# Performance work log

Measured on AMD Instinct MI355X. Metric: run time of the kernel, lower is better.

Reference implementation:

```python
import jax, jax.numpy as jnp
import numpy as np

B, S, H, NH = 2, 2048, 1024, 16
HD = H // NH            # 64
ROT = HD // 2           # rotary dim = 32
COND, FF = 1024, 4 * H
BASE = 10000.0
EPS = 1e-5


def setup_inputs() -> dict:
    key = jax.random.key(0)
    ks = jax.random.split(key, 16)
    w = lambda k, shape: jax.random.normal(k, shape, dtype=jnp.float32) * 0.02
    z = lambda shape: jnp.zeros(shape, dtype=jnp.float32)
    o = lambda shape: jnp.ones(shape, dtype=jnp.float32)
    return {
        'x': jax.random.normal(ks[0], (B, S, H), dtype=jnp.float32),
        'cond': jax.random.normal(ks[1], (B, COND), dtype=jnp.float32),
        'attn_mask': jnp.ones((B, S), dtype=bool),
        'wq': w(ks[2], (H, H)), 'bq': z((H,)),
        'wk': w(ks[3], (H, H)), 'bk': z((H,)),
        'wv': w(ks[4], (H, H)), 'bv': z((H,)),
        'wo': w(ks[5], (H, H)), 'bo': z((H,)),
        'ln1_g': o((H,)), 'ln1_b': z((H,)),
        'ada1_w': w(ks[6], (COND, 2 * H)), 'ada1_b': z((2 * H,)),
        'ln2_g': o((H,)), 'ln2_b': z((H,)),
        'ada2_w': w(ks[7], (COND, 2 * H)), 'ada2_b': z((2 * H,)),
        'ff_w1': w(ks[8], (H, FF)), 'ff_b1': z((FF,)),
        'ff_w2': w(ks[9], (FF, H)), 'ff_b2': z((H,)),
    }


def _layer_norm(x, g, b):
    mu = jnp.mean(x, axis=-1, keepdims=True)
    var = jnp.mean(jnp.square(x - mu), axis=-1, keepdims=True)
    return (x - mu) * jax.lax.rsqrt(var + EPS) * g + b


def _ada_norm(x, cond, g, b, w, bw):
    shift, scale = jnp.split(cond @ w + bw, 2, axis=-1)  # each [B,H]
    return _layer_norm(x, g, b) * (1.0 + scale[:, None, :]) + shift[:, None, :]


def _rotary_sin_cos(seq_len):
    inv_freq = 1.0 / (BASE ** (jnp.arange(ROT, dtype=jnp.float32) / ROT))
    freqs = jnp.arange(seq_len, dtype=jnp.float32)[:, None] * inv_freq[None, :]  # [S,ROT]
    return jnp.sin(freqs), jnp.cos(freqs)


def _apply_rotary(x, sin, cos):
    # x: [B,NH,S,HD]; sin/cos: [S,ROT] broadcast over batch/heads
    xe, xo = x[..., ::2], x[..., 1::2]
    re = xe * cos - xo * sin
    ro = xo * cos + xe * sin
    return jnp.stack((re, ro), axis=-1).reshape(x.shape)


def _split_heads(x):
    b, s, _ = x.shape
    return x.reshape(b, s, NH, HD).transpose(0, 2, 1, 3)  # [B,NH,S,HD]


def reference(x, cond, attn_mask, wq, bq, wk, bk, wv, bv, wo, bo,
              ln1_g, ln1_b, ada1_w, ada1_b, ln2_g, ln2_b, ada2_w, ada2_b,
              ff_w1, ff_b1, ff_w2, ff_b2):
    residual = x
    h = _ada_norm(x, cond, ln1_g, ln1_b, ada1_w, ada1_b)
    q = _split_heads(h @ wq + bq)
    k = _split_heads(h @ wk + bk)
    v = _split_heads(h @ wv + bv)
    sin, cos = _rotary_sin_cos(x.shape[1])
    q = _apply_rotary(q, sin, cos)
    k = _apply_rotary(k, sin, cos)
    scores = jnp.einsum('bhqd,bhkd->bhqk', q, k) / np.sqrt(HD).astype(np.float32)
    scores = jnp.where(attn_mask[:, None, None, :], scores, -jnp.inf)
    attn = jax.nn.softmax(scores, axis=-1)
    out = jnp.einsum('bhqk,bhkd->bhqd', attn, v)
    out = out.transpose(0, 2, 1, 3).reshape(x.shape[0], x.shape[1], H)
    x = residual + out @ wo + bo
    residual = x
    h = _ada_norm(x, cond, ln2_g, ln2_b, ada2_w, ada2_b)
    ff = jax.nn.gelu(h @ ff_w1 + ff_b1, approximate=False) @ ff_w2 + ff_b2
    return residual + ff
```

## Files before the change

### kernel.cpp

```cpp
#include <hip/hip_runtime.h>
#include <cstdint>

#define B_DIM 2
#define S_DIM 2048
#define H_DIM 1024
#define NHEAD 16
#define HDIM 64
#define FF_DIM 4096
#define M_DIM (B_DIM*S_DIM)

typedef __bf16 bf16;
typedef _Float16 f16;
typedef __bf16 bf16x8 __attribute__((ext_vector_type(8)));
typedef __bf16 bf16x4 __attribute__((ext_vector_type(4)));
typedef _Float16 f16x4 __attribute__((ext_vector_type(4)));
typedef __fp16 fp16x2_raw __attribute__((ext_vector_type(2)));
typedef float  f32x4  __attribute__((ext_vector_type(4)));

#define QK_SCALE 0.18033688011112042f

#if __has_builtin(__builtin_amdgcn_exp2f)
#define EXP2F(x) __builtin_amdgcn_exp2f(x)
#else
#define EXP2F(x) __expf(0.69314718055994531f*(x))
#endif

#define ATOMIC_FADD(p, v) __hip_atomic_fetch_add((p), (v), __ATOMIC_RELAXED, __HIP_MEMORY_SCOPE_AGENT)

__device__ __forceinline__ void g2l16(void* lds, const void* g) {
    __builtin_amdgcn_global_load_lds(
        (const __attribute__((address_space(1))) void*)g,
        (__attribute__((address_space(3))) void*)lds,
        16, 0, 0);
}

__global__ __launch_bounds__(256) void wtrans_all(const float* __restrict__ wq,
                                                  const float* __restrict__ wk,
                                                  const float* __restrict__ wv,
                                                  const float* __restrict__ wo,
                                                  const float* __restrict__ fw1,
                                                  const float* __restrict__ fw2,
                                                  bf16* __restrict__ wqkv,
                                                  bf16* __restrict__ wto,
                                                  bf16* __restrict__ wtf1,
                                                  bf16* __restrict__ wtf2,
                                                  float* __restrict__ adao) {
    __shared__ float t[32][33];
    int tt = blockIdx.x;
    if (tt >= 12288) {
        int i = (tt - 12288) * 1024 + threadIdx.x * 4;
        ((float4*)(adao + i))[0] = (float4){0.f, 0.f, 0.f, 0.f};
        return;
    }
    const float* in; bf16* out; int R, C, base, shift;
    if (tt < 4096) {
        int j = tt >> 10; base = tt & 1023; R = 1024; C = 1024; shift = 5;
        in  = (j == 0) ? wq : (j == 1) ? wk : (j == 2) ? wv : wo;
        out = (j < 3) ? (wqkv + (size_t)j * 1024 * 1024) : wto;
    } else if (tt < 8192) {
        base = tt - 4096; R = 1024; C = 4096; shift = 7; in = fw1; out = wtf1;
    } else {
        base = tt - 8192; R = 4096; C = 1024; shift = 5; in = fw2; out = wtf2;
    }
    int bx = base & ((1 << shift) - 1), by = base >> shift;
    int c0 = bx * 32, r0 = by * 32;
    int tx = threadIdx.x & 31, ty = threadIdx.x >> 5;
#pragma unroll
    for (int i = 0; i < 4; i++) {
        int r = ty + i * 8;
        t[r][tx] = in[(size_t)(r0 + r) * C + c0 + tx];
    }
    __syncthreads();
#pragma unroll
    for (int i = 0; i < 4; i++) {
        int cc = ty + i * 8;
        out[(size_t)(c0 + cc) * R + r0 + tx] = (bf16)t[tx][cc];
    }
}

__global__ __launch_bounds__(256) void ada_gemm(const float* __restrict__ cond,
                                                const float* __restrict__ w1, const float* __restrict__ b1,
                                                const float* __restrict__ w2, const float* __restrict__ b2,
                                                float* __restrict__ o1, float* __restrict__ o2) {
    int layer = blockIdx.y;
    const float* w    = layer ? w2 : w1;
    const float* bias = layer ? b2 : b1;
    float* o          = layer ? o2 : o1;
    int tid = threadIdx.x;
    int k0 = blockIdx.x * 16;
    f32x4 acc[2][2];
#pragma unroll
    for (int b = 0; b < 2; b++)
#pragma unroll
        for (int j = 0; j < 2; j++) acc[b][j] = (f32x4){0.f, 0.f, 0.f, 0.f};

#pragma unroll
    for (int kk = 0; kk < 16; kk++) {
        int k = k0 + kk;
        float c0 = cond[k];
        float c1 = cond[1024 + k];
        const f32x4* wr = (const f32x4*)(w + (size_t)k * 2048);
        f32x4 wa = wr[tid], wb = wr[tid + 256];
#pragma unroll
        for (int c = 0; c < 4; c++) {
            acc[0][0][c] += c0 * wa[c];
            acc[0][1][c] += c0 * wb[c];
            acc[1][0][c] += c1 * wa[c];
            acc[1][1][c] += c1 * wb[c];
        }
    }
    if (blockIdx.x == 0) {
        f32x4 ba = ((const f32x4*)bias)[tid], bb = ((const f32x4*)bias)[tid + 256];
#pragma unroll
        for (int c = 0; c < 4; c++) {
            acc[0][0][c] += ba[c]; acc[1][0][c] += ba[c];
            acc[0][1][c] += bb[c]; acc[1][1][c] += bb[c];
        }
    }
#pragma unroll
    for (int b = 0; b < 2; b++)
#pragma unroll
        for (int j = 0; j < 2; j++) {
            int col = (tid + j * 256) * 4;
#pragma unroll
            for (int c = 0; c < 4; c++)
                ATOMIC_FADD(&o[b * 2048 + col + c], acc[b][j][c]);
        }
}

__global__ __launch_bounds__(256) void adaln_k(const float* __restrict__ x,
                                               const float* __restrict__ g,
                                               const float* __restrict__ be,
                                               const float* __restrict__ ada,
                                               bf16* __restrict__ h) {
    int row = blockIdx.x;
    int b = row >> 11;
    int tid = threadIdx.x;
    float4 v = ((const float4*)(x + (size_t)row * H_DIM))[tid];
    float s = v.x + v.y + v.z + v.w;
    __shared__ float sm[4];
#pragma unroll
    for (int m = 32; m >= 1; m >>= 1) s += __shfl_xor(s, m, 64);
    if ((tid & 63) == 0) sm[tid >> 6] = s;
    __syncthreads();
    float mean = (sm[0] + sm[1] + sm[2] + sm[3]) * (1.0f / H_DIM);
    float dx = v.x - mean, dy = v.y - mean, dz = v.z - mean, dw = v.w - mean;
    float s2 = dx * dx + dy * dy + dz * dz + dw * dw;
    __syncthreads();
#pragma unroll
    for (int m = 32; m >= 1; m >>= 1) s2 += __shfl_xor(s2, m, 64);
    if ((tid & 63) == 0) sm[tid >> 6] = s2;
    __syncthreads();
    float var = (sm[0] + sm[1] + sm[2] + sm[3]) * (1.0f / H_DIM);
    float rstd = rsqrtf(var + 1e-5f);
    float4 gv = ((const float4*)g)[tid];
    float4 bv = ((const float4*)be)[tid];
    const float* shp = ada + (size_t)b * 2 * H_DIM;
    float4 shv = ((const float4*)shp)[tid];
    float4 scv = ((const float4*)(shp + H_DIM))[tid];
    bf16* hr = h + (size_t)row * H_DIM + tid * 4;
    hr[0] = (bf16)((dx * rstd * gv.x + bv.x) * (1.0f + scv.x) + shv.x);
    hr[1] = (bf16)((dy * rstd * gv.y + bv.y) * (1.0f + scv.y) + shv.y);
    hr[2] = (bf16)((dz * rstd * gv.z + bv.z) * (1.0f + scv.z) + shv.z);
    hr[3] = (bf16)((dw * rstd * gv.w + bv.w) * (1.0f + scv.w) + shv.w);
}

__global__ __launch_bounds__(256) void adaln2_fused(const float* __restrict__ x,
                                                    const float* __restrict__ bo,
                                                    const bf16* __restrict__ P0,
                                                    const bf16* __restrict__ P1,
                                                    const float* __restrict__ g,
                                                    const float* __restrict__ be,
                                                    const float* __restrict__ ada,
                                                    float* __restrict__ x2,
                                                    bf16* __restrict__ h) {
    int row = blockIdx.x;
    int b = row >> 11;
    int tid = threadIdx.x;
    float4 v = ((const float4*)(x + (size_t)row * H_DIM))[tid];
    float4 bov = ((const float4*)bo)[tid];
    bf16x4 p0 = ((const bf16x4*)(P0 + (size_t)row * H_DIM))[tid];
    bf16x4 p1 = ((const bf16x4*)(P1 + (size_t)row * H_DIM))[tid];
    v.x += bov.x + (float)p0[0] + (float)p1[0];
    v.y += bov.y + (float)p0[1] + (float)p1[1];
    v.z += bov.z + (float)p0[2] + (float)p1[2];
    v.w += bov.w + (float)p0[3] + (float)p1[3];
    ((float4*)(x2 + (size_t)row * H_DIM))[tid] = v;

    float s = v.x + v.y + v.z + v.w;
    __shared__ float sm[4];
#pragma unroll
    for (int m = 32; m >= 1; m >>= 1) s += __shfl_xor(s, m, 64);
    if ((tid & 63) == 0) sm[tid >> 6] = s;
    __syncthreads();
    float mean = (sm[0] + sm[1] + sm[2] + sm[3]) * (1.0f / H_DIM);
    float dx = v.x - mean, dy = v.y - mean, dz = v.z - mean, dw = v.w - mean;
    float s2 = dx * dx + dy * dy + dz * dz + dw * dw;
    __syncthreads();
#pragma unroll
    for (int m = 32; m >= 1; m >>= 1) s2 += __shfl_xor(s2, m, 64);
    if ((tid & 63) == 0) sm[tid >> 6] = s2;
    __syncthreads();
    float var = (sm[0] + sm[1] + sm[2] + sm[3]) * (1.0f / H_DIM);
    float rstd = rsqrtf(var + 1e-5f);
    float4 gv = ((const float4*)g)[tid];
    float4 bv = ((const float4*)be)[tid];
    const float* shp = ada + (size_t)b * 2 * H_DIM;
    float4 shv = ((const float4*)shp)[tid];
    float4 scv = ((const float4*)(shp + H_DIM))[tid];
    bf16* hr = h + (size_t)row * H_DIM + tid * 4;
    hr[0] = (bf16)((dx * rstd * gv.x + bv.x) * (1.0f + scv.x) + shv.x);
    hr[1] = (bf16)((dy * rstd * gv.y + bv.y) * (1.0f + scv.y) + shv.y);
    hr[2] = (bf16)((dz * rstd * gv.z + bv.z) * (1.0f + scv.z) + shv.z);
    hr[3] = (bf16)((dw * rstd * gv.w + bv.w) * (1.0f + scv.w) + shv.w);
}

__global__ __launch_bounds__(256) void final_reduce(const float* __restrict__ x2,
                                                    const float* __restrict__ fb2,
                                                    const bf16* __restrict__ Q,
                                                    float* __restrict__ out) {
    int i = blockIdx.x * 256 + threadIdx.x;
    float4 v = ((const float4*)x2)[i];
    float4 bv = ((const float4*)fb2)[i & 255];
    v.x += bv.x; v.y += bv.y; v.z += bv.z; v.w += bv.w;
#pragma unroll
    for (int z = 0; z < 4; z++) {
        bf16x4 q = ((const bf16x4*)(Q + (size_t)z * M_DIM * H_DIM))[i];
        v.x += (float)q[0]; v.y += (float)q[1]; v.z += (float)q[2]; v.w += (float)q[3];
    }
    ((float4*)out)[i] = v;
}

__global__ __launch_bounds__(256, 2) void gemm_bt_sp(const bf16* __restrict__ A,
                                                     const bf16* __restrict__ Bt,
                                                     bf16* __restrict__ outp,
                                                     int N, int K, int KC) {
    __shared__ bf16 As[128 * 32];
    __shared__ bf16 Bs[128 * 32];
    int m0 = blockIdx.y * 128, n0 = blockIdx.x * 128;
    int kbeg = blockIdx.z * KC, kend = kbeg + KC;
    bf16* po = outp + (size_t)blockIdx.z * M_DIM * N;
    int tid = threadIdx.x, wid = tid >> 6, lane = tid & 63;
    int quad = lane >> 4, l16 = lane & 15;
    int wm = (wid >> 1) * 64, wn = (wid & 1) * 64;

    f32x4 acc[4][4];
#pragma unroll
    for (int i = 0; i < 4; i++)
#pragma unroll
        for (int j = 0; j < 4; j++) acc[i][j] = (f32x4){0.f, 0.f, 0.f, 0.f};

    for (int k0 = kbeg; k0 < kend; k0 += 32) {
        __syncthreads();
#pragma unroll
        for (int it = 0; it < 2; it++) {
            int c = it * 256 + wid * 64 + lane;
            int row = c >> 2, kc = c & 3;
            g2l16(&As[c * 8], A  + (size_t)(m0 + row) * K + k0 + kc * 8);
            g2l16(&Bs[c * 8], Bt + (size_t)(n0 + row) * K + k0 + kc * 8);
        }
        __syncthreads();
        bf16x8 af[4], bfr[4];
#pragma unroll
        for (int i = 0; i < 4; i++) {
            af[i]  = *(const bf16x8*)&As[(wm + i * 16 + l16) * 32 + quad * 8];
            bfr[i] = *(const bf16x8*)&Bs[(wn + i * 16 + l16) * 32 + quad * 8];
        }
#pragma unroll
        for (int mt = 0; mt < 4; mt++)
#pragma unroll
            for (int nt = 0; nt < 4; nt++)
                acc[mt][nt] = __builtin_amdgcn_mfma_f32_16x16x32_bf16(af[mt], bfr[nt], acc[mt][nt], 0, 0, 0);
    }

#pragma unroll
    for (int mt = 0; mt < 4; mt++) {
#pragma unroll
        for (int nt = 0; nt < 4; nt++) {
            int col = n0 + wn + nt * 16 + l16;
#pragma unroll
            for (int r = 0; r < 4; r++) {
                int row = m0 + wm + mt * 16 + quad * 4 + r;
                po[(size_t)row * N + col] = (bf16)acc[mt][nt][r];
            }
        }
    }
}

__global__ __launch_bounds__(256, 2) void gemm_gelu(const bf16* __restrict__ A,
                                                    const bf16* __restrict__ Bt,
                                                    const float* __restrict__ bias,
                                                    bf16* __restrict__ outp,
                                                    int N, int K) {
    __shared__ bf16 As[128 * 32];
    __shared__ bf16 Bs[128 * 32];
    int m0 = blockIdx.y * 128, n0 = blockIdx.x * 128;
    int tid = threadIdx.x, wid = tid >> 6, lane = tid & 63;
    int quad = lane >> 4, l16 = lane & 15;
    int wm = (wid >> 1) * 64, wn = (wid & 1) * 64;

    f32x4 acc[4][4];
#pragma unroll
    for (int i = 0; i < 4; i++)
#pragma unroll
        for (int j = 0; j < 4; j++) acc[i][j] = (f32x4){0.f, 0.f, 0.f, 0.f};

    for (int k0 = 0; k0 < K; k0 += 32) {
        __syncthreads();
#pragma unroll
        for (int it = 0; it < 2; it++) {
            int c = it * 256 + wid * 64 + lane;
            int row = c >> 2, kc = c & 3;
            g2l16(&As[c * 8], A  + (size_t)(m0 + row) * K + k0 + kc * 8);
            g2l16(&Bs[c * 8], Bt + (size_t)(n0 + row) * K + k0 + kc * 8);
        }
        __syncthreads();
        bf16x8 af[4], bfr[4];
#pragma unroll
        for (int i = 0; i < 4; i++) {
            af[i]  = *(const bf16x8*)&As[(wm + i * 16 + l16) * 32 + quad * 8];
            bfr[i] = *(const bf16x8*)&Bs[(wn + i * 16 + l16) * 32 + quad * 8];
        }
#pragma unroll
        for (int mt = 0; mt < 4; mt++)
#pragma unroll
            for (int nt = 0; nt < 4; nt++)
                acc[mt][nt] = __builtin_amdgcn_mfma_f32_16x16x32_bf16(af[mt], bfr[nt], acc[mt][nt], 0, 0, 0);
    }

#pragma unroll
    for (int mt = 0; mt < 4; mt++) {
#pragma unroll
        for (int nt = 0; nt < 4; nt++) {
            int col = n0 + wn + nt * 16 + l16;
            float bc = bias[col];
#pragma unroll
            for (int r = 0; r < 4; r++) {
                int row = m0 + wm + mt * 16 + quad * 4 + r;
                float v = acc[mt][nt][r] + bc;
                float gl = 0.5f * v * (1.0f + erff(v * 0.70710678118654752f));
                outp[(size_t)row * N + col] = (bf16)gl;
            }
        }
    }
}

__global__ __launch_bounds__(256, 2) void gemm_qkv(const bf16* __restrict__ A,
                                                   const bf16* __restrict__ Bt,
                                                   const float* __restrict__ bq,
                                                   const float* __restrict__ bk,
                                                   const float* __restrict__ bv,
                                                   bf16* __restrict__ qr,
                                                   bf16* __restrict__ kr,
                                                   f16* __restrict__ vtf) {
    __shared__ bf16 As[128 * 32];
    __shared__ bf16 Bs[128 * 32];
    const int K = H_DIM;
    int m0 = blockIdx.y * 128, n0 = blockIdx.x * 128;
    int tid = threadIdx.x, wid = tid >> 6, lane = tid & 63;
    int quad = lane >> 4, l16 = lane & 15;
    int wm = (wid >> 1) * 64, wn = (wid & 1) * 64;

    f32x4 acc[4][4];
#pragma unroll
    for (int i = 0; i < 4; i++)
#pragma unroll
        for (int j = 0; j < 4; j++) acc[i][j] = (f32x4){0.f, 0.f, 0.f, 0.f};

    for (int k0 = 0; k0 < K; k0 += 32) {
        __syncthreads();
#pragma unroll
        for (int it = 0; it < 2; it++) {
            int c = it * 256 + wid * 64 + lane;
            int row = c >> 2, kc = c & 3;
            g2l16(&As[c * 8], A  + (size_t)(m0 + row) * K + k0 + kc * 8);
            g2l16(&Bs[c * 8], Bt + (size_t)(n0 + row) * K + k0 + kc * 8);
        }
        __syncthreads();
        bf16x8 af[4], bfr[4];
#pragma unroll
        for (int i = 0; i < 4; i++) {
            af[i]  = *(const bf16x8*)&As[(wm + i * 16 + l16) * 32 + quad * 8];
            bfr[i] = *(const bf16x8*)&Bs[(wn + i * 16 + l16) * 32 + quad * 8];
        }
#pragma unroll
        for (int mt = 0; mt < 4; mt++)
#pragma unroll
            for (int nt = 0; nt < 4; nt++)
                acc[mt][nt] = __builtin_amdgcn_mfma_f32_16x16x32_bf16(af[mt], bfr[nt], acc[mt][nt], 0, 0, 0);
    }

#pragma unroll
    for (int mt = 0; mt < 4; mt++) {
#pragma unroll
        for (int nt = 0; nt < 4; nt++) {
            int col = n0 + wn + nt * 16 + l16;
            int sec = col >> 10;
            int cc  = col & 1023;
            float bc = (sec == 0) ? bq[cc] : (sec == 1) ? bk[cc] : bv[cc];
            int hh = cc >> 6, d = cc & 63;
#pragma unroll
            for (int r = 0; r < 4; r++) {
                int row = m0 + wm + mt * 16 + quad * 4 + r;
                int bb = row >> 11, s = row & (S_DIM - 1);
                float v = acc[mt][nt][r] + bc;
                if (sec < 2) {
                    float pv = __shfl_xor(v, 1, 64);
                    int i2 = d >> 1;
                    float ang = (float)s * __expf(-0.2878231366242676f * (float)i2);
                    float sn = __sinf(ang), cs = __cosf(ang);
                    float nv = (d & 1) ? (v * cs + pv * sn) : (v * cs - pv * sn);
                    if (sec == 0) nv *= QK_SCALE;
                    bf16* dst = sec ? kr : qr;
                    dst[(((size_t)(bb * NHEAD + hh)) * S_DIM + s) * HDIM + d] = (bf16)nv;
                } else {
                    vtf[(((size_t)(bb * NHEAD + hh)) * HDIM + d) * S_DIM + s] = (f16)v;
                }
            }
        }
    }
}

__global__ __launch_bounds__(128, 4) void flash(const bf16* __restrict__ Q,
                                                const bf16* __restrict__ Kg,
                                                const f16* __restrict__ Vt,
                                                bf16* __restrict__ O) {
    int bh = blockIdx.x;
    int q0 = blockIdx.y * 64;
    int b = bh >> 4, h = bh & (NHEAD - 1);
    int tid = threadIdx.x, wid = tid >> 6, lane = tid & 63;
    int quad = lane >> 4, l16 = lane & 15;
    int j3 = l16 & 7;

    __shared__ bf16 Ks[128 * 64];
    __shared__ f16  Vs[64 * 128];

    const bf16* Qb = Q  + ((size_t)bh * S_DIM + q0 + wid * 32) * HDIM;
    const bf16* Kb = Kg + (size_t)bh * S_DIM * HDIM;
    const f16*  Vb = Vt + (size_t)bh * HDIM * S_DIM;

    bf16x8 qf[2][2];
#pragma unroll
    for (int qt = 0; qt < 2; qt++)
#pragma unroll
        for (int ks = 0; ks < 2; ks++)
            qf[qt][ks] = *(const bf16x8*)(Qb + (size_t)(qt * 16 + l16) * HDIM + ks * 32 + quad * 8);

    f32x4 oacc[4][2];
#pragma unroll
    for (int i = 0; i < 4; i++)
#pragma unroll
        for (int j = 0; j < 2; j++) oacc[i][j] = (f32x4){0.f, 0.f, 0.f, 0.f};
    float lsum[2] = {0.f, 0.f};

    for (int kt = 0; kt < S_DIM; kt += 128) {
        __syncthreads();
#pragma unroll
        for (int it = 0; it < 8; it++) {
            int c = it * 128 + tid;
            int krow = c >> 3, kp = c & 7;
            g2l16(&Ks[c * 8], Kb + (size_t)(kt + krow) * HDIM + (kp ^ (krow & 7)) * 8);
            int vrow = c >> 4, vp = c & 15;
            g2l16(&Vs[c * 8], Vb + (size_t)vrow * S_DIM + kt + ((vp ^ (vrow & 7)) * 8));
        }
        __syncthreads();

        f32x4 sacc[8][2];
#pragma unroll
        for (int i = 0; i < 8; i++)
#pragma unroll
            for (int j = 0; j < 2; j++) sacc[i][j] = (f32x4){0.f, 0.f, 0.f, 0.f};
#pragma unroll
        for (int nt = 0; nt < 8; nt++)
#pragma unroll
            for (int ks = 0; ks < 2; ks++) {
                int row = nt * 16 + l16;
                int pc = (ks * 4 + quad) ^ j3;
                bf16x8 kf = *(const bf16x8*)&Ks[row * 64 + pc * 8];
#pragma unroll
                for (int qt = 0; qt < 2; qt++)
                    sacc[nt][qt] = __builtin_amdgcn_mfma_f32_16x16x32_bf16(kf, qf[qt][ks], sacc[nt][qt], 0, 0, 0);
            }

#pragma unroll
        for (int qt = 0; qt < 2; qt++) {
            float rs = 0.f;
#pragma unroll
            for (int nt = 0; nt < 8; nt++)
#pragma unroll
                for (int r = 0; r < 4; r++) {
                    float p = EXP2F(sacc[nt][qt][r]);
                    sacc[nt][qt][r] = p;
                    rs += p;
                }
            lsum[qt] += rs;
        }

#pragma unroll
        for (int kc = 0; kc < 8; kc++) {
            f16x4 pf[2];
#pragma unroll
            for (int qt = 0; qt < 2; qt++) {
                union { fp16x2_raw h2[2]; f16x4 h4; } u;
                u.h2[0] = __builtin_amdgcn_cvt_pkrtz(sacc[kc][qt][0], sacc[kc][qt][1]);
                u.h2[1] = __builtin_amdgcn_cvt_pkrtz(sacc[kc][qt][2], sacc[kc][qt][3]);
                pf[qt] = u.h4;
            }
#pragma unroll
            for (int mt = 0; mt < 4; mt++) {
                int row = mt * 16 + l16;
                int pc = (2 * kc + (quad >> 1)) ^ j3;
                f16x4 vf = *(const f16x4*)&Vs[row * 128 + pc * 8 + (quad & 1) * 4];
#pragma unroll
                for (int qt = 0; qt < 2; qt++)
                    oacc[mt][qt] = __builtin_amdgcn_mfma_f32_16x16x16f16(vf, pf[qt], oacc[mt][qt], 0, 0, 0);
            }
        }
    }

    float inv[2];
#pragma unroll
    for (int qt = 0; qt < 2; qt++) {
        float l = lsum[qt];
        l += __shfl_xor(l, 16, 64);
        l += __shfl_xor(l, 32, 64);
        inv[qt] = 1.0f / l;
    }
#pragma unroll
    for (int mt = 0; mt < 4; mt++)
#pragma unroll
        for (int qt = 0; qt < 2; qt++) {
            int q = q0 + wid * 32 + qt * 16 + l16;
            int d = mt * 16 + quad * 4;
            bf16x4 o;
#pragma unroll
            for (int r = 0; r < 4; r++) o[r] = (bf16)(oacc[mt][qt][r] * inv[qt]);
            *(bf16x4*)(O + ((size_t)b * S_DIM + q) * H_DIM + h * HDIM + d) = o;
        }
}

extern "C" void kernel_launch(void* const* d_in, const int* in_sizes, int n_in,
                              void* d_out, int out_size, void* d_ws, size_t ws_size,
                              hipStream_t stream) {
    const float* x     = (const float*)d_in[0];
    const float* cond  = (const float*)d_in[1];
    const float* wq    = (const float*)d_in[3];
    const float* bq    = (const float*)d_in[4];
    const float* wk    = (const float*)d_in[5];
    const float* bk    = (const float*)d_in[6];
    const float* wv    = (const float*)d_in[7];
    const float* bv    = (const float*)d_in[8];
    const float* wo    = (const float*)d_in[9];
    const float* bo    = (const float*)d_in[10];
    const float* ln1g  = (const float*)d_in[11];
    const float* ln1b  = (const float*)d_in[12];
    const float* ada1w = (const float*)d_in[13];
    const float* ada1b = (const float*)d_in[14];
    const float* ln2g  = (const float*)d_in[15];
    const float* ln2b  = (const float*)d_in[16];
    const float* ada2w = (const float*)d_in[17];
    const float* ada2b = (const float*)d_in[18];
    const float* fw1   = (const float*)d_in[19];
    const float* fb1   = (const float*)d_in[20];
    const float* fw2   = (const float*)d_in[21];
    const float* fb2   = (const float*)d_in[22];

    char* p = (char*)d_ws;
    auto take = [&](size_t n) { char* r = p; p += (n + 255) & ~(size_t)255; return (void*)r; };

    bf16* wqkv = (bf16*)take((size_t)3 * H_DIM * H_DIM * 2);
    bf16* wto  = (bf16*)take((size_t)H_DIM * H_DIM * 2);
    bf16* wtf1 = (bf16*)take((size_t)FF_DIM * H_DIM * 2);
    bf16* wtf2 = (bf16*)take((size_t)H_DIM * FF_DIM * 2);
    float* adao  = (float*)take((size_t)2 * B_DIM * 2 * H_DIM * 4);
    float* ada1o = adao;
    float* ada2o = adao + (size_t)B_DIM * 2 * H_DIM;
    bf16* h    = (bf16*)take((size_t)M_DIM * H_DIM * 2);
    bf16* qr   = (bf16*)take((size_t)M_DIM * H_DIM * 2);
    bf16* kr   = (bf16*)take((size_t)M_DIM * H_DIM * 2);
    f16*  vtf  = (f16*) take((size_t)M_DIM * H_DIM * 2);
    bf16* attn = (bf16*)take((size_t)M_DIM * H_DIM * 2);
    float* x2  = (float*)take((size_t)M_DIM * H_DIM * 4);
    bf16* Qp   = (bf16*)take((size_t)4 * M_DIM * H_DIM * 2);
    bf16* Pp   = Qp;
    bf16* ff1b = qr;

    wtrans_all<<<12290, 256, 0, stream>>>(wq, wk, wv, wo, fw1, fw2,
                                          wqkv, wto, wtf1, wtf2, adao);

    ada_gemm<<<dim3(64, 2), 256, 0, stream>>>(cond, ada1w, ada1b, ada2w, ada2b, ada1o, ada2o);
    adaln_k<<<M_DIM, 256, 0, stream>>>(x, ln1g, ln1b, ada1o, h);

    gemm_qkv<<<dim3(24, 32), 256, 0, stream>>>(h, wqkv, bq, bk, bv, qr, kr, vtf);

    flash<<<dim3(32, 32), 128, 0, stream>>>(qr, kr, vtf, attn);

    gemm_bt_sp<<<dim3(8, 32, 2), 256, 0, stream>>>(attn, wto, Pp, H_DIM, H_DIM, H_DIM / 2);
    adaln2_fused<<<M_DIM, 256, 0, stream>>>(x, bo, Pp, Pp + (size_t)M_DIM * H_DIM,
                                            ln2g, ln2b, ada2o, x2, h);

    gemm_gelu<<<dim3(32, 32), 256, 0, stream>>>(h, wtf1, fb1, ff1b, FF_DIM, H_DIM);

    gemm_bt_sp<<<dim3(8, 32, 4), 256, 0, stream>>>(ff1b, wtf2, Qp, H_DIM, FF_DIM, FF_DIM / 4);
    final_reduce<<<M_DIM * H_DIM / 1024, 256, 0, stream>>>(x2, fb2, Qp, (float*)d_out);

    (void)in_sizes; (void)n_in; (void)out_size; (void)ws_size;
}
```

Measured before the change: 423.0 us.

## Use K64 swizzled GEMM tiles and split flash attention across key halves

The three MFMA GEMM kernels now stage 64-wide K tiles in LDS with an XOR swizzle. That halves the barriers per K step and is meant to avoid LDS bank conflicts. The flash kernel now runs 256-thread blocks of 128 queries and splits the key range into two halves along grid z. Each half writes unnormalized partial outputs and row sums, and a new attn_combine kernel adds them and normalizes. This trades extra memory traffic and a launch for different parallelism and occupancy, and doubles the LDS footprint in the GEMMs.

```diff
diff --git a/kernel.cpp b/kernel.cpp
--- a/kernel.cpp
+++ b/kernel.cpp
@@ -235,8 +235,8 @@
                                                      const bf16* __restrict__ Bt,
                                                      bf16* __restrict__ outp,
                                                      int N, int K, int KC) {
-    __shared__ bf16 As[128 * 32];
-    __shared__ bf16 Bs[128 * 32];
+    __shared__ bf16 As[128 * 64];
+    __shared__ bf16 Bs[128 * 64];
     int m0 = blockIdx.y * 128, n0 = blockIdx.x * 128;
     int kbeg = blockIdx.z * KC, kend = kbeg + KC;
     bf16* po = outp + (size_t)blockIdx.z * M_DIM * N;
@@ -250,27 +250,33 @@
 #pragma unroll
         for (int j = 0; j < 4; j++) acc[i][j] = (f32x4){0.f, 0.f, 0.f, 0.f};
 
-    for (int k0 = kbeg; k0 < kend; k0 += 32) {
-        __syncthreads();
-#pragma unroll
-        for (int it = 0; it < 2; it++) {
-            int c = it * 256 + wid * 64 + lane;
-            int row = c >> 2, kc = c & 3;
-            g2l16(&As[c * 8], A  + (size_t)(m0 + row) * K + k0 + kc * 8);
-            g2l16(&Bs[c * 8], Bt + (size_t)(n0 + row) * K + k0 + kc * 8);
-        }
-        __syncthreads();
-        bf16x8 af[4], bfr[4];
-#pragma unroll
-        for (int i = 0; i < 4; i++) {
-            af[i]  = *(const bf16x8*)&As[(wm + i * 16 + l16) * 32 + quad * 8];
-            bfr[i] = *(const bf16x8*)&Bs[(wn + i * 16 + l16) * 32 + quad * 8];
-        }
-#pragma unroll
-        for (int mt = 0; mt < 4; mt++)
-#pragma unroll
-            for (int nt = 0; nt < 4; nt++)
-                acc[mt][nt] = __builtin_amdgcn_mfma_f32_16x16x32_bf16(af[mt], bfr[nt], acc[mt][nt], 0, 0, 0);
+    for (int k0 = kbeg; k0 < kend; k0 += 64) {
+        __syncthreads();
+#pragma unroll
+        for (int it = 0; it < 4; it++) {
+            int c = it * 256 + tid;
+            int row = c >> 3, kp = c & 7;
+            int sc = (kp ^ (row & 7)) * 8;
+            g2l16(&As[c * 8], A  + (size_t)(m0 + row) * K + k0 + sc);
+            g2l16(&Bs[c * 8], Bt + (size_t)(n0 + row) * K + k0 + sc);
+        }
+        __syncthreads();
+#pragma unroll
+        for (int ks = 0; ks < 2; ks++) {
+            bf16x8 af[4], bfr[4];
+#pragma unroll
+            for (int i = 0; i < 4; i++) {
+                int ra = wm + i * 16 + l16;
+                int rb = wn + i * 16 + l16;
+                af[i]  = *(const bf16x8*)&As[ra * 64 + (((ks * 4 + quad) ^ (ra & 7)) * 8)];
+                bfr[i] = *(const bf16x8*)&Bs[rb * 64 + (((ks * 4 + quad) ^ (rb & 7)) * 8)];
+            }
+#pragma unroll
+            for (int mt = 0; mt < 4; mt++)
+#pragma unroll
+                for (int nt = 0; nt < 4; nt++)
+                    acc[mt][nt] = __builtin_amdgcn_mfma_f32_16x16x32_bf16(af[mt], bfr[nt], acc[mt][nt], 0, 0, 0);
+        }
     }
 
 #pragma unroll
@@ -292,8 +298,8 @@
                                                     const float* __restrict__ bias,
                                                     bf16* __restrict__ outp,
                                                     int N, int K) {
-    __shared__ bf16 As[128 * 32];
-    __shared__ bf16 Bs[128 * 32];
+    __shared__ bf16 As[128 * 64];
+    __shared__ bf16 Bs[128 * 64];
     int m0 = blockIdx.y * 128, n0 = blockIdx.x * 128;
     int tid = threadIdx.x, wid = tid >> 6, lane = tid & 63;
     int quad = lane >> 4, l16 = lane & 15;
@@ -305,27 +311,33 @@
 #pragma unroll
         for (int j = 0; j < 4; j++) acc[i][j] = (f32x4){0.f, 0.f, 0.f, 0.f};
 
-    for (int k0 = 0; k0 < K; k0 += 32) {
-        __syncthreads();
-#pragma unroll
-        for (int it = 0; it < 2; it++) {
-            int c = it * 256 + wid * 64 + lane;
-            int row = c >> 2, kc = c & 3;
-            g2l16(&As[c * 8], A  + (size_t)(m0 + row) * K + k0 + kc * 8);
-            g2l16(&Bs[c * 8], Bt + (size_t)(n0 + row) * K + k0 + kc * 8);
-        }
-        __syncthreads();
-        bf16x8 af[4], bfr[4];
-#pragma unroll
-        for (int i = 0; i < 4; i++) {
-            af[i]  = *(const bf16x8*)&As[(wm + i * 16 + l16) * 32 + quad * 8];
-            bfr[i] = *(const bf16x8*)&Bs[(wn + i * 16 + l16) * 32 + quad * 8];
-        }
-#pragma unroll
-        for (int mt = 0; mt < 4; mt++)
-#pragma unroll
-            for (int nt = 0; nt < 4; nt++)
-                acc[mt][nt] = __builtin_amdgcn_mfma_f32_16x16x32_bf16(af[mt], bfr[nt], acc[mt][nt], 0, 0, 0);
+    for (int k0 = 0; k0 < K; k0 += 64) {
+        __syncthreads();
+#pragma unroll
+        for (int it = 0; it < 4; it++) {
+            int c = it * 256 + tid;
+            int row = c >> 3, kp = c & 7;
+            int sc = (kp ^ (row & 7)) * 8;
+            g2l16(&As[c * 8], A  + (size_t)(m0 + row) * K + k0 + sc);
+            g2l16(&Bs[c * 8], Bt + (size_t)(n0 + row) * K + k0 + sc);
+        }
+        __syncthreads();
+#pragma unroll
+        for (int ks = 0; ks < 2; ks++) {
+            bf16x8 af[4], bfr[4];
+#pragma unroll
+            for (int i = 0; i < 4; i++) {
+                int ra = wm + i * 16 + l16;
+                int rb = wn + i * 16 + l16;
+                af[i]  = *(const bf16x8*)&As[ra * 64 + (((ks * 4 + quad) ^ (ra & 7)) * 8)];
+                bfr[i] = *(const bf16x8*)&Bs[rb * 64 + (((ks * 4 + quad) ^ (rb & 7)) * 8)];
+            }
+#pragma unroll
+            for (int mt = 0; mt < 4; mt++)
+#pragma unroll
+                for (int nt = 0; nt < 4; nt++)
+                    acc[mt][nt] = __builtin_amdgcn_mfma_f32_16x16x32_bf16(af[mt], bfr[nt], acc[mt][nt], 0, 0, 0);
+        }
     }
 
 #pragma unroll
@@ -353,8 +365,8 @@
                                                    bf16* __restrict__ qr,
                                                    bf16* __restrict__ kr,
                                                    f16* __restrict__ vtf) {
-    __shared__ bf16 As[128 * 32];
-    __shared__ bf16 Bs[128 * 32];
+    __shared__ bf16 As[128 * 64];
+    __shared__ bf16 Bs[128 * 64];
     const int K = H_DIM;
     int m0 = blockIdx.y * 128, n0 = blockIdx.x * 128;
     int tid = threadIdx.x, wid = tid >> 6, lane = tid & 63;
@@ -367,27 +379,33 @@
 #pragma unroll
         for (int j = 0; j < 4; j++) acc[i][j] = (f32x4){0.f, 0.f, 0.f, 0.f};
 
-    for (int k0 = 0; k0 < K; k0 += 32) {
-        __syncthreads();
-#pragma unroll
-        for (int it = 0; it < 2; it++) {
-            int c = it * 256 + wid * 64 + lane;
-            int row = c >> 2, kc = c & 3;
-            g2l16(&As[c * 8], A  + (size_t)(m0 + row) * K + k0 + kc * 8);
-            g2l16(&Bs[c * 8], Bt + (size_t)(n0 + row) * K + k0 + kc * 8);
-        }
-        __syncthreads();
-        bf16x8 af[4], bfr[4];
-#pragma unroll
-        for (int i = 0; i < 4; i++) {
-            af[i]  = *(const bf16x8*)&As[(wm + i * 16 + l16) * 32 + quad * 8];
-            bfr[i] = *(const bf16x8*)&Bs[(wn + i * 16 + l16) * 32 + quad * 8];
-        }
-#pragma unroll
-        for (int mt = 0; mt < 4; mt++)
-#pragma unroll
-            for (int nt = 0; nt < 4; nt++)
-                acc[mt][nt] = __builtin_amdgcn_mfma_f32_16x16x32_bf16(af[mt], bfr[nt], acc[mt][nt], 0, 0, 0);
+    for (int k0 = 0; k0 < K; k0 += 64) {
+        __syncthreads();
+#pragma unroll
+        for (int it = 0; it < 4; it++) {
+            int c = it * 256 + tid;
+            int row = c >> 3, kp = c & 7;
+            int sc = (kp ^ (row & 7)) * 8;
+            g2l16(&As[c * 8], A  + (size_t)(m0 + row) * K + k0 + sc);
+            g2l16(&Bs[c * 8], Bt + (size_t)(n0 + row) * K + k0 + sc);
+        }
+        __syncthreads();
+#pragma unroll
+        for (int ks = 0; ks < 2; ks++) {
+            bf16x8 af[4], bfr[4];
+#pragma unroll
+            for (int i = 0; i < 4; i++) {
+                int ra = wm + i * 16 + l16;
+                int rb = wn + i * 16 + l16;
+                af[i]  = *(const bf16x8*)&As[ra * 64 + (((ks * 4 + quad) ^ (ra & 7)) * 8)];
+                bfr[i] = *(const bf16x8*)&Bs[rb * 64 + (((ks * 4 + quad) ^ (rb & 7)) * 8)];
+            }
+#pragma unroll
+            for (int mt = 0; mt < 4; mt++)
+#pragma unroll
+                for (int nt = 0; nt < 4; nt++)
+                    acc[mt][nt] = __builtin_amdgcn_mfma_f32_16x16x32_bf16(af[mt], bfr[nt], acc[mt][nt], 0, 0, 0);
+        }
     }
 
 #pragma unroll
@@ -421,12 +439,14 @@
     }
 }
 
-__global__ __launch_bounds__(128, 4) void flash(const bf16* __restrict__ Q,
+__global__ __launch_bounds__(256, 2) void flash(const bf16* __restrict__ Q,
                                                 const bf16* __restrict__ Kg,
                                                 const f16* __restrict__ Vt,
-                                                bf16* __restrict__ O) {
+                                                bf16* __restrict__ Op,
+                                                float* __restrict__ Ls) {
     int bh = blockIdx.x;
-    int q0 = blockIdx.y * 64;
+    int q0 = blockIdx.y * 128;
+    int z  = blockIdx.z;
     int b = bh >> 4, h = bh & (NHEAD - 1);
     int tid = threadIdx.x, wid = tid >> 6, lane = tid & 63;
     int quad = lane >> 4, l16 = lane & 15;
@@ -453,11 +473,11 @@
         for (int j = 0; j < 2; j++) oacc[i][j] = (f32x4){0.f, 0.f, 0.f, 0.f};
     float lsum[2] = {0.f, 0.f};
 
-    for (int kt = 0; kt < S_DIM; kt += 128) {
-        __syncthreads();
-#pragma unroll
-        for (int it = 0; it < 8; it++) {
-            int c = it * 128 + tid;
+    for (int kt = z * (S_DIM / 2); kt < (z + 1) * (S_DIM / 2); kt += 128) {
+        __syncthreads();
+#pragma unroll
+        for (int it = 0; it < 4; it++) {
+            int c = it * 256 + tid;
             int krow = c >> 3, kp = c & 7;
             g2l16(&Ks[c * 8], Kb + (size_t)(kt + krow) * HDIM + (kp ^ (krow & 7)) * 8);
             int vrow = c >> 4, vp = c & 15;
@@ -518,14 +538,15 @@
         }
     }
 
-    float inv[2];
 #pragma unroll
     for (int qt = 0; qt < 2; qt++) {
         float l = lsum[qt];
         l += __shfl_xor(l, 16, 64);
         l += __shfl_xor(l, 32, 64);
-        inv[qt] = 1.0f / l;
-    }
+        if (quad == 0)
+            Ls[(size_t)z * 32 * S_DIM + bh * S_DIM + q0 + wid * 32 + qt * 16 + l16] = l;
+    }
+    bf16* Oz = Op + (size_t)z * M_DIM * H_DIM;
 #pragma unroll
     for (int mt = 0; mt < 4; mt++)
 #pragma unroll
@@ -534,9 +555,28 @@
             int d = mt * 16 + quad * 4;
             bf16x4 o;
 #pragma unroll
-            for (int r = 0; r < 4; r++) o[r] = (bf16)(oacc[mt][qt][r] * inv[qt]);
-            *(bf16x4*)(O + ((size_t)b * S_DIM + q) * H_DIM + h * HDIM + d) = o;
-        }
+            for (int r = 0; r < 4; r++) o[r] = (bf16)oacc[mt][qt][r];
+            *(bf16x4*)(Oz + ((size_t)b * S_DIM + q) * H_DIM + h * HDIM + d) = o;
+        }
+}
+
+__global__ __launch_bounds__(256) void attn_combine(const bf16* __restrict__ Op,
+                                                    const float* __restrict__ Ls,
+                                                    bf16* __restrict__ attn) {
+    int row = blockIdx.x;
+    int b = row >> 11, s = row & (S_DIM - 1);
+    int tid = threadIdx.x;
+    int h = tid >> 4;
+    float l0 = Ls[(size_t)(b * NHEAD + h) * S_DIM + s];
+    float l1 = Ls[(size_t)32 * S_DIM + (size_t)(b * NHEAD + h) * S_DIM + s];
+    float inv = 1.0f / (l0 + l1);
+    size_t i = (size_t)row * 256 + tid;
+    bf16x4 a = ((const bf16x4*)Op)[i];
+    bf16x4 c = ((const bf16x4*)(Op + (size_t)M_DIM * H_DIM))[i];
+    bf16x4 o;
+#pragma unroll
+    for (int r = 0; r < 4; r++) o[r] = (bf16)(((float)a[r] + (float)c[r]) * inv);
+    ((bf16x4*)attn)[i] = o;
 }
 
 extern "C" void kernel_launch(void* const* d_in, const int* in_sizes, int n_in,
@@ -581,7 +621,9 @@
     f16*  vtf  = (f16*) take((size_t)M_DIM * H_DIM * 2);
     bf16* attn = (bf16*)take((size_t)M_DIM * H_DIM * 2);
     float* x2  = (float*)take((size_t)M_DIM * H_DIM * 4);
+    float* Ls  = (float*)take((size_t)2 * 32 * S_DIM * 4);
     bf16* Qp   = (bf16*)take((size_t)4 * M_DIM * H_DIM * 2);
+    bf16* Op   = Qp;
     bf16* Pp   = Qp;
     bf16* ff1b = qr;
 
@@ -593,7 +635,8 @@
 
     gemm_qkv<<<dim3(24, 32), 256, 0, stream>>>(h, wqkv, bq, bk, bv, qr, kr, vtf);
 
-    flash<<<dim3(32, 32), 128, 0, stream>>>(qr, kr, vtf, attn);
+    flash<<<dim3(32, 16, 2), 256, 0, stream>>>(qr, kr, vtf, Op, Ls);
+    attn_combine<<<M_DIM, 256, 0, stream>>>(Op, Ls, attn);
 
     gemm_bt_sp<<<dim3(8, 32, 2), 256, 0, stream>>>(attn, wto, Pp, H_DIM, H_DIM, H_DIM / 2);
     adaln2_fused<<<M_DIM, 256, 0, stream>>>(x, bo, Pp, Pp + (size_t)M_DIM * H_DIM,
```

After: 391.5 us. 1.08x faster.
